# Optimization experiments

Hardware: AMD Instinct MI355X
Metric: run time of the kernel (lower is better)

Reference implementation:

```python
import jax, jax.numpy as jnp
import numpy as np

N, M, K, D = 65536, 131072, 8, 64
TAU = 0.3
EPS = 1e-6

def setup_inputs() -> dict:
    key = jax.random.key(0)
    ks = jax.random.split(key, 16)
    s = 0.05
    return {
        "f_pts": jax.random.normal(ks[0], (N, D), jnp.float32),
        "pts": jax.random.uniform(ks[1], (N, 3), jnp.float32) * 10.0,
        "z_latent": jax.random.normal(ks[2], (M, D), jnp.float32) * 0.1,
        "centers": jax.random.uniform(ks[3], (M, 3), jnp.float32) * 10.0,
        "cand_idx": jax.random.randint(ks[4], (N, K), 0, M),
        "sim_w1": jax.random.normal(ks[5], (2 * D + 3, 64), jnp.float32) * s,
        "sim_b1": jnp.zeros((64,), jnp.float32),
        "sim_w2": jax.random.normal(ks[6], (64, 1), jnp.float32) * s,
        "sim_b2": jnp.zeros((1,), jnp.float32),
        "gate_w1": jax.random.normal(ks[7], (2 * D, D), jnp.float32) * s,
        "gate_b1": jnp.zeros((D,), jnp.float32),
        "gate_w2": jax.random.normal(ks[8], (D, 1), jnp.float32) * s,
        "gate_b2": jnp.zeros((1,), jnp.float32),
        "W_ih": jax.random.normal(ks[9], (3 * D, D), jnp.float32) * s,
        "W_hh": jax.random.normal(ks[10], (3 * D, D), jnp.float32) * s,
        "b_ih": jnp.zeros((3 * D,), jnp.float32),
        "b_hh": jnp.zeros((3 * D,), jnp.float32),
    }

def _forward(f_pts, pts, z_latent, centers, sim_w1, sim_b1, sim_w2, sim_b2,
             gate_w1, gate_b1, gate_w2, gate_b2, W_ih, W_hh, b_ih, b_hh, cand_idx):
    n, k = cand_idx.shape
    m, d = z_latent.shape
    # --- gather voxel latents / centers for each (point, candidate) pair ---
    z_c = z_latent[cand_idx]                         # (N,K,D)
    delta = pts[:, None, :] - centers[cand_idx]      # (N,K,3)
    f_b = jnp.broadcast_to(f_pts[:, None, :], (n, k, d))
    # --- similarity MLP ---
    x = jnp.concatenate([f_b, z_c, delta], axis=-1)  # (N,K,2D+3)
    h = jax.nn.relu(x @ sim_w1 + sim_b1)
    sim = (h @ sim_w2 + sim_b2)[..., 0]              # (N,K)
    # --- low-temperature top-K routing weights over candidates ---
    w = jax.nn.softmax(sim / TAU, axis=-1)           # (N,K)
    # --- scatter weighted point features to voxels ---
    flat_idx = cand_idx.reshape(-1)                  # (N*K,)
    contrib = (w[..., None] * f_pts[:, None, :]).reshape(-1, d)
    msg = jax.ops.segment_sum(contrib, flat_idx, num_segments=m)     # (M,D)
    wsum = jax.ops.segment_sum(w.reshape(-1), flat_idx, num_segments=m)
    msg = msg / (wsum[:, None] + EPS)                # normalized voxel message
    # --- per-voxel gate ---
    g_in = jnp.concatenate([z_latent, msg], axis=-1)
    gate = jax.nn.sigmoid(jax.nn.relu(g_in @ gate_w1 + gate_b1) @ gate_w2 + gate_b2)  # (M,1)
    # --- GRUCell (torch layout: rows ordered r,z,n) ---
    gi = msg @ W_ih.T + b_ih
    gh = z_latent @ W_hh.T + b_hh
    i_r, i_z, i_n = jnp.split(gi, 3, axis=-1)
    h_r, h_z, h_n = jnp.split(gh, 3, axis=-1)
    r = jax.nn.sigmoid(i_r + h_r)
    zg = jax.nn.sigmoid(i_z + h_z)
    nn_ = jnp.tanh(i_n + r * h_n)
    h_new = (1.0 - zg) * nn_ + zg * z_latent
    # gated latent update
    return z_latent + gate * (h_new - z_latent)

def reference(f_pts, pts, z_latent, centers, cand_idx, sim_w1, sim_b1, sim_w2, sim_b2,
              gate_w1, gate_b1, gate_w2, gate_b2, W_ih, W_hh, b_ih, b_hh):
    return _forward(f_pts, pts, z_latent, centers, sim_w1, sim_b1, sim_w2, sim_b2,
                    gate_w1, gate_b1, gate_w2, gate_b2, W_ih, W_hh, b_ih, b_hh, cand_idx)
```

## Files before the change

### kernel.cpp

```cpp
#include <hip/hip_runtime.h>
#include <hip/hip_fp16.h>
#include <math.h>


typedef short bf16x8 __attribute__((ext_vector_type(8)));
typedef unsigned short u16x8 __attribute__((ext_vector_type(8)));
typedef float f32x4 __attribute__((ext_vector_type(4)));
#define MFMA __builtin_amdgcn_mfma_f32_16x16x32_bf16
#define CAP 32

__device__ __forceinline__ short f2bf(float f) {
  unsigned u = __float_as_uint(f);
  unsigned r = (u + 0x7FFFu + ((u >> 16) & 1u)) >> 16;
  return (short)r;
}

__device__ __forceinline__ float bf2f(unsigned short h) {
  return __uint_as_float(((unsigned)h) << 16);
}

__device__ __forceinline__ float sigm(float x) { return 1.0f / (1.0f + __expf(-x)); }

__global__ __launch_bounds__(256) void prep_kernel(
    const float* __restrict__ z, const float* __restrict__ f,
    const float* __restrict__ sim_w1, const float* __restrict__ sim_b1,
    unsigned short* __restrict__ zbf, unsigned short* __restrict__ fbf,
    unsigned short* __restrict__ HBt, int* __restrict__ cursor,
    short* __restrict__ bfZ, int M)
{
  long tid = (long)blockIdx.x * 256 + threadIdx.x;
  long nthr = (long)gridDim.x * 256;

  for (long i = tid; i < M; i += nthr) cursor[i] = 0;

  long nz = (long)M * 64;
  for (long i = tid * 8; i < nz; i += nthr * 8) {
    float4 a = *(const float4*)&z[i];
    float4 b4 = *(const float4*)&z[i + 4];
    u16x8 o;
    o[0] = (unsigned short)f2bf(a.x);  o[1] = (unsigned short)f2bf(a.y);
    o[2] = (unsigned short)f2bf(a.z);  o[3] = (unsigned short)f2bf(a.w);
    o[4] = (unsigned short)f2bf(b4.x); o[5] = (unsigned short)f2bf(b4.y);
    o[6] = (unsigned short)f2bf(b4.z); o[7] = (unsigned short)f2bf(b4.w);
    *(u16x8*)&zbf[i] = o;
  }

  if (blockIdx.x == gridDim.x - 1 && threadIdx.x < 64) {
    int lane = threadIdx.x;
    int lr = lane & 15, lg = lane >> 4;
#pragma unroll
    for (int ct = 0; ct < 4; ++ct)
#pragma unroll
      for (int kt = 0; kt < 3; ++kt) {
        bf16x8 b;
#pragma unroll
        for (int e = 0; e < 8; ++e) {
          int k = kt * 32 + lg * 8 + e;
          float v = (k < 67) ? sim_w1[(64 + k) * 64 + ct * 16 + lr] : 0.0f;
          b[e] = f2bf(v);
        }
        *(bf16x8*)&bfZ[(ct * 3 + kt) * 512 + lane * 8] = b;
      }
  }

  if (blockIdx.x < 1024) {
    int wave = blockIdx.x * 4 + (threadIdx.x >> 6);
    int lane = threadIdx.x & 63;
    int lr = lane & 15, lg = lane >> 4;
    int n0 = wave * 16;

    bf16x8 bf[8];
#pragma unroll
    for (int ct = 0; ct < 4; ++ct)
#pragma unroll
      for (int kt = 0; kt < 2; ++kt) {
        bf16x8 bb;
#pragma unroll
        for (int e = 0; e < 8; ++e)
          bb[e] = f2bf(sim_w1[(kt * 32 + lg * 8 + e) * 64 + ct * 16 + lr]);
        bf[ct * 2 + kt] = bb;
      }

    bf16x8 a[2];
#pragma unroll
    for (int kt = 0; kt < 2; ++kt) {
      const float* src = &f[(long)(n0 + lr) * 64 + kt * 32 + lg * 8];
      float4 v0 = *(const float4*)src;
      float4 v1 = *(const float4*)(src + 4);
      bf16x8 t;
      t[0] = f2bf(v0.x); t[1] = f2bf(v0.y); t[2] = f2bf(v0.z); t[3] = f2bf(v0.w);
      t[4] = f2bf(v1.x); t[5] = f2bf(v1.y); t[6] = f2bf(v1.z); t[7] = f2bf(v1.w);
      a[kt] = t;
    }
    *(bf16x8*)&fbf[(long)(n0 + lr) * 64 + lg * 8] = a[0];
    *(bf16x8*)&fbf[(long)(n0 + lr) * 64 + 32 + lg * 8] = a[1];

    f32x4 acc[4] = {{0,0,0,0},{0,0,0,0},{0,0,0,0},{0,0,0,0}};
#pragma unroll
    for (int ct = 0; ct < 4; ++ct) {
      acc[ct] = MFMA(a[0], bf[ct * 2 + 0], acc[ct], 0, 0, 0);
      acc[ct] = MFMA(a[1], bf[ct * 2 + 1], acc[ct], 0, 0, 0);
    }
    float b10 = sim_b1[lr], b11 = sim_b1[16 + lr];
    float b12 = sim_b1[32 + lr], b13 = sim_b1[48 + lr];
#pragma unroll
    for (int e = 0; e < 4; ++e) {
      unsigned lo = (unsigned)(unsigned short)f2bf(acc[0][e] + b10)
                  | ((unsigned)(unsigned short)f2bf(acc[1][e] + b11) << 16);
      unsigned hi = (unsigned)(unsigned short)f2bf(acc[2][e] + b12)
                  | ((unsigned)(unsigned short)f2bf(acc[3][e] + b13) << 16);
      *(uint2*)&HBt[(long)(n0 + lg * 4 + e) * 64 + lr * 4] = make_uint2(lo, hi);
    }
  }
}

#define TPW 8
__global__ __launch_bounds__(256) void pair_kernel(
    const float* __restrict__ pts, const unsigned short* __restrict__ zbf,
    const float* __restrict__ centers, const int* __restrict__ cand_idx,
    const float* __restrict__ sim_w2, const short* __restrict__ bfZ,
    const unsigned short* __restrict__ HBt,
    int* __restrict__ cursor, unsigned* __restrict__ rec)
{
  int wave = (blockIdx.x * 256 + threadIdx.x) >> 6;
  int lane = threadIdx.x & 63;
  int lr = lane & 15, lg = lane >> 4;

  int callA = cand_idx[wave * 128 + lane];
  int callB = cand_idx[wave * 128 + 64 + lane];
  int slotA = atomicAdd(&cursor[callA], 1);
  int slotB = atomicAdd(&cursor[callB], 1);

  bf16x8 b[12];
#pragma unroll
  for (int i = 0; i < 12; ++i) b[i] = *(const bf16x8*)&bfZ[i * 512 + lane * 8];
  float w2c[4];
#pragma unroll
  for (int ct = 0; ct < 4; ++ct) w2c[ct] = sim_w2[ct * 16 + lr];

  int c0 = __shfl(callA, lr, 64);
  bf16x8 a0 = *(const bf16x8*)&zbf[(long)c0 * 64 + lg * 8];
  bf16x8 a1 = *(const bf16x8*)&zbf[(long)c0 * 64 + 32 + lg * 8];
  float cx = 0, cy = 0, cz = 0, px = 0, py = 0, pz = 0;
  if (lg == 0) {
    cx = centers[c0 * 3 + 0]; cy = centers[c0 * 3 + 1]; cz = centers[c0 * 3 + 2];
    int n = wave * TPW * 2 + (lr >> 3);
    px = pts[n * 3 + 0]; py = pts[n * 3 + 1]; pz = pts[n * 3 + 2];
  }
  uint2 h2 = *(const uint2*)&HBt[((long)wave * TPW * 2 + (lg >> 1)) * 64 + lr * 4];

  float wst[TPW];

#pragma unroll
  for (int t = 0; t < TPW; ++t) {
    int cn = c0; bf16x8 an0 = a0, an1 = a1;
    float cxn = 0, cyn = 0, czn = 0, pxn = 0, pyn = 0, pzn = 0;
    uint2 h2n = make_uint2(0, 0);
    if (t + 1 < TPW) {
      cn = __shfl((t + 1) < 4 ? callA : callB, ((t + 1) & 3) * 16 + lr, 64);
      an0 = *(const bf16x8*)&zbf[(long)cn * 64 + lg * 8];
      an1 = *(const bf16x8*)&zbf[(long)cn * 64 + 32 + lg * 8];
      if (lg == 0) {
        cxn = centers[cn * 3 + 0]; cyn = centers[cn * 3 + 1]; czn = centers[cn * 3 + 2];
        int n = (wave * TPW + t + 1) * 2 + (lr >> 3);
        pxn = pts[n * 3 + 0]; pyn = pts[n * 3 + 1]; pzn = pts[n * 3 + 2];
      }
      h2n = *(const uint2*)&HBt[((long)(wave * TPW + t + 1) * 2 + (lg >> 1)) * 64 + lr * 4];
    }

    bf16x8 ad = {0, 0, 0, 0, 0, 0, 0, 0};
    if (lg == 0) {
      ad[0] = f2bf(px - cx); ad[1] = f2bf(py - cy); ad[2] = f2bf(pz - cz);
    }

    f32x4 acc[4] = {{0,0,0,0},{0,0,0,0},{0,0,0,0},{0,0,0,0}};
#pragma unroll
    for (int ct = 0; ct < 4; ++ct) {
      acc[ct] = MFMA(a0, b[ct * 3 + 0], acc[ct], 0, 0, 0);
      acc[ct] = MFMA(a1, b[ct * 3 + 1], acc[ct], 0, 0, 0);
      acc[ct] = MFMA(ad, b[ct * 3 + 2], acc[ct], 0, 0, 0);
    }

    float hb[4];
    hb[0] = bf2f((unsigned short)(h2.x));
    hb[1] = bf2f((unsigned short)(h2.x >> 16));
    hb[2] = bf2f((unsigned short)(h2.y));
    hb[3] = bf2f((unsigned short)(h2.y >> 16));

    f32x4 part = {0.f, 0.f, 0.f, 0.f};
#pragma unroll
    for (int ct = 0; ct < 4; ++ct)
#pragma unroll
      for (int e = 0; e < 4; ++e) {
        float u = fmaxf(acc[ct][e] + hb[ct], 0.0f);
        part[e] = fmaf(u, w2c[ct], part[e]);
      }
#pragma unroll
    for (int m = 1; m <= 8; m <<= 1)
#pragma unroll
      for (int e = 0; e < 4; ++e) part[e] += __shfl_xor(part[e], m, 64);

    float other[4];
#pragma unroll
    for (int e = 0; e < 4; ++e) other[e] = __shfl_xor(part[e], 16, 64);

    float mx = part[0];
#pragma unroll
    for (int e = 1; e < 4; ++e) mx = fmaxf(mx, part[e]);
#pragma unroll
    for (int e = 0; e < 4; ++e) mx = fmaxf(mx, other[e]);
    float ex[4], se = 0.f, so = 0.f;
#pragma unroll
    for (int e = 0; e < 4; ++e) {
      ex[e] = __expf((part[e] - mx) * (1.0f / 0.3f));
      se += ex[e];
      so += __expf((other[e] - mx) * (1.0f / 0.3f));
    }
    float inv = 1.0f / (se + so);

    int srcl = (lane >> 2) << 4;
    float t0 = __shfl(ex[0] * inv, srcl, 64);
    float t1 = __shfl(ex[1] * inv, srcl, 64);
    float t2 = __shfl(ex[2] * inv, srcl, 64);
    float t3 = __shfl(ex[3] * inv, srcl, 64);
    int esel = lane & 3;
    wst[t] = esel == 0 ? t0 : esel == 1 ? t1 : esel == 2 ? t2 : t3;

    c0 = cn; a0 = an0; a1 = an1;
    cx = cxn; cy = cyn; cz = czn; px = pxn; py = pyn; pz = pzn;
    h2 = h2n;
  }

  float v0 = __shfl(wst[0], lr, 64);
  float v1 = __shfl(wst[1], lr, 64);
  float v2 = __shfl(wst[2], lr, 64);
  float v3 = __shfl(wst[3], lr, 64);
  float v4 = __shfl(wst[4], lr, 64);
  float v5 = __shfl(wst[5], lr, 64);
  float v6 = __shfl(wst[6], lr, 64);
  float v7 = __shfl(wst[7], lr, 64);
  float wvA = lg == 0 ? v0 : lg == 1 ? v1 : lg == 2 ? v2 : v3;
  float wvB = lg == 0 ? v4 : lg == 1 ? v5 : lg == 2 ? v6 : v7;

  int base_pt = wave * 16 + 2 * lg + (lr >> 3);
  if (slotA < CAP) {
    unsigned short wh = __half_as_ushort(__float2half(wvA));
    rec[(long)callA * CAP + slotA] = ((unsigned)base_pt << 16) | (unsigned)wh;
  }
  if (slotB < CAP) {
    unsigned short wh = __half_as_ushort(__float2half(wvB));
    rec[(long)callB * CAP + slotB] = ((unsigned)(base_pt + 8) << 16) | (unsigned)wh;
  }
}

__global__ __launch_bounds__(256) void gather_kernel(
    const unsigned* __restrict__ rec, const int* __restrict__ cursor,
    const unsigned short* __restrict__ fbf, unsigned short* __restrict__ msg_bf,
    int mvox)
{
  int tid = blockIdx.x * 256 + threadIdx.x;
  int row = tid >> 2, seg = tid & 3;
  if (row >= mvox) return;

  int cnt = cursor[row];
  cnt = cnt < CAP ? cnt : CAP;
  const unsigned* rp = &rec[(long)row * CAP];

  float acc[16];
#pragma unroll
  for (int j = 0; j < 16; ++j) acc[j] = 0.f;
  float ws = 0.f;

  for (int i0 = 0; i0 < cnt; i0 += 4) {
    uint4 r4 = *(const uint4*)&rp[i0];
    unsigned rr0 = r4.x, rr1 = r4.y, rr2 = r4.z, rr3 = r4.w;
#pragma unroll
    for (int j = 0; j < 4; ++j) {
      unsigned r = j == 0 ? rr0 : j == 1 ? rr1 : j == 2 ? rr2 : rr3;
      if (i0 + j < cnt) {
        float w = __half2float(__ushort_as_half((unsigned short)(r & 0xffffu)));
        int n = r >> 16;
        ws += w;
        const u16x8* fp = (const u16x8*)&fbf[(long)n * 64 + seg * 16];
        u16x8 f0 = fp[0], f1 = fp[1];
#pragma unroll
        for (int k = 0; k < 8; ++k) {
          acc[k]     = fmaf(w, bf2f(f0[k]), acc[k]);
          acc[8 + k] = fmaf(w, bf2f(f1[k]), acc[8 + k]);
        }
      }
    }
  }
  float inv = 1.0f / (ws + 1e-6f);
  u16x8 o0, o1;
#pragma unroll
  for (int j = 0; j < 8; ++j) {
    o0[j] = (unsigned short)f2bf(acc[j] * inv);
    o1[j] = (unsigned short)f2bf(acc[8 + j] * inv);
  }
  *(u16x8*)&msg_bf[(long)row * 64 + seg * 16] = o0;
  *(u16x8*)&msg_bf[(long)row * 64 + seg * 16 + 8] = o1;
}

#define GST 136
#define WST 72

__global__ __launch_bounds__(512)
__attribute__((amdgpu_waves_per_eu(2, 2)))
void stage2(
    const unsigned short* __restrict__ zbf,
    const float* __restrict__ gate_w1, const float* __restrict__ gate_b1,
    const float* __restrict__ gate_w2, const float* __restrict__ gate_b2,
    const float* __restrict__ W_ih, const float* __restrict__ W_hh,
    const float* __restrict__ b_ih, const float* __restrict__ b_hh,
    const unsigned short* __restrict__ msg_bf,
    float* __restrict__ out, int ntiles)
{
  __shared__ short G1t[64 * GST];
  __shared__ short Wih_l[192 * WST];
  __shared__ short Whh_l[192 * WST];
  __shared__ float gb1s[64], gw2s[64], bihs[192], bhhs[192];
  __shared__ float gb2s;

  int t = threadIdx.x;
  for (int s = t; s < 64 * 128; s += 512) {
    int j = s & 63, k = s >> 6;
    G1t[j * GST + k] = f2bf(gate_w1[s]);
  }
  for (int s = t; s < 192 * 64; s += 512) {
    int j = s >> 6, k = s & 63;
    Wih_l[j * WST + k] = f2bf(W_ih[s]);
    Whh_l[j * WST + k] = f2bf(W_hh[s]);
  }
  if (t < 64) { gb1s[t] = gate_b1[t]; gw2s[t] = gate_w2[t]; }
  if (t < 192) { bihs[t] = b_ih[t]; bhhs[t] = b_hh[t]; }
  if (t == 0) gb2s = gate_b2[0];
  __syncthreads();

  int wid = t >> 6, lane = t & 63;
  int lr = lane & 15, lg = lane >> 4;

#pragma unroll 1
  for (int tile = blockIdx.x; tile < ntiles; tile += gridDim.x) {
    int rowbase = tile * 128 + wid * 16;
    long abase = (long)(rowbase + lr) * 64;
    bf16x8 a0 = *(const bf16x8*)&zbf[abase + lg * 8];
    bf16x8 a1 = *(const bf16x8*)&zbf[abase + 32 + lg * 8];
    bf16x8 a2 = *(const bf16x8*)&msg_bf[abase + lg * 8];
    bf16x8 a3 = *(const bf16x8*)&msg_bf[abase + 32 + lg * 8];

    f32x4 usum = {0.f, 0.f, 0.f, 0.f};
#pragma unroll 1
    for (int ct = 0; ct < 4; ++ct) {
      f32x4 au = {0, 0, 0, 0};
      au = MFMA(a0, *(const bf16x8*)&G1t[(ct * 16 + lr) * GST +  0 + lg * 8], au, 0, 0, 0);
      au = MFMA(a1, *(const bf16x8*)&G1t[(ct * 16 + lr) * GST + 32 + lg * 8], au, 0, 0, 0);
      au = MFMA(a2, *(const bf16x8*)&G1t[(ct * 16 + lr) * GST + 64 + lg * 8], au, 0, 0, 0);
      au = MFMA(a3, *(const bf16x8*)&G1t[(ct * 16 + lr) * GST + 96 + lg * 8], au, 0, 0, 0);
      int c = ct * 16 + lr;
#pragma unroll
      for (int e = 0; e < 4; ++e)
        usum[e] += fmaxf(au[e] + gb1s[c], 0.0f) * gw2s[c];
    }
#pragma unroll
    for (int m = 1; m <= 8; m <<= 1)
#pragma unroll
      for (int e = 0; e < 4; ++e) {
        float v = usum[e];
        usum[e] = v + __shfl_xor(v, m, 64);
      }
    float gate[4];
#pragma unroll
    for (int e = 0; e < 4; ++e) gate[e] = sigm(usum[e] + gb2s);

#pragma unroll 1
    for (int ct = 0; ct < 4; ++ct) {
      f32x4 air = {0,0,0,0}, aiz = {0,0,0,0}, ain = {0,0,0,0};
      f32x4 ahr = {0,0,0,0}, ahz = {0,0,0,0}, ahn = {0,0,0,0};
#pragma unroll
      for (int k2 = 0; k2 < 2; ++k2) {
        bf16x8 amg = k2 ? a3 : a2;
        bf16x8 az_ = k2 ? a1 : a0;
        int ko = k2 * 32 + lg * 8;
        air = MFMA(amg, *(const bf16x8*)&Wih_l[(      ct * 16 + lr) * WST + ko], air, 0, 0, 0);
        aiz = MFMA(amg, *(const bf16x8*)&Wih_l[( 64 + ct * 16 + lr) * WST + ko], aiz, 0, 0, 0);
        ain = MFMA(amg, *(const bf16x8*)&Wih_l[(128 + ct * 16 + lr) * WST + ko], ain, 0, 0, 0);
        ahr = MFMA(az_, *(const bf16x8*)&Whh_l[(      ct * 16 + lr) * WST + ko], ahr, 0, 0, 0);
        ahz = MFMA(az_, *(const bf16x8*)&Whh_l[( 64 + ct * 16 + lr) * WST + ko], ahz, 0, 0, 0);
        ahn = MFMA(az_, *(const bf16x8*)&Whh_l[(128 + ct * 16 + lr) * WST + ko], ahn, 0, 0, 0);
      }
      int c = ct * 16 + lr;
#pragma unroll
      for (int e = 0; e < 4; ++e) {
        float zv = bf2f(zbf[(long)(rowbase + lg * 4 + e) * 64 + c]);
        float rr = sigm(air[e] + bihs[c] + ahr[e] + bhhs[c]);
        float zg = sigm(aiz[e] + bihs[64 + c] + ahz[e] + bhhs[64 + c]);
        float nn = tanhf(ain[e] + bihs[128 + c] + rr * (ahn[e] + bhhs[128 + c]));
        float hnew = (1.0f - zg) * nn + zg * zv;
        out[(long)(rowbase + lg * 4 + e) * 64 + c] = zv + gate[e] * (hnew - zv);
      }
    }
  }
}

extern "C" void kernel_launch(void* const* d_in, const int* in_sizes, int n_in,
                              void* d_out, int out_size, void* d_ws, size_t ws_size,
                              hipStream_t stream) {
  const float* f_pts   = (const float*)d_in[0];
  const float* pts     = (const float*)d_in[1];
  const float* z_lat   = (const float*)d_in[2];
  const float* centers = (const float*)d_in[3];
  const int*   cand    = (const int*)d_in[4];
  const float* sim_w1  = (const float*)d_in[5];
  const float* sim_b1  = (const float*)d_in[6];
  const float* sim_w2  = (const float*)d_in[7];
  const float* gate_w1 = (const float*)d_in[9];
  const float* gate_b1 = (const float*)d_in[10];
  const float* gate_w2 = (const float*)d_in[11];
  const float* gate_b2 = (const float*)d_in[12];
  const float* W_ih    = (const float*)d_in[13];
  const float* W_hh    = (const float*)d_in[14];
  const float* b_ih    = (const float*)d_in[15];
  const float* b_hh    = (const float*)d_in[16];

  int N = in_sizes[0] / 64;
  int M = in_sizes[2] / 64;

  int* cursor = (int*)d_ws;
  unsigned* rec = (unsigned*)(cursor + M);
  unsigned short* msg_bf = (unsigned short*)rec;
  unsigned short* zbf = (unsigned short*)(rec + (size_t)M * CAP);
  unsigned short* fbf = zbf + (size_t)M * 64;
  unsigned short* HBt = fbf + (size_t)N * 64;
  short* bfZ = (short*)(HBt + (size_t)N * 64);

  prep_kernel<<<2048, 256, 0, stream>>>(z_lat, f_pts, sim_w1, sim_b1,
                                        zbf, fbf, HBt, cursor, bfZ, M);

  int nwaves = (N * 8) / (16 * TPW);
  pair_kernel<<<nwaves / 4, 256, 0, stream>>>(pts, zbf, centers, cand,
                                              sim_w2, bfZ, HBt, cursor, rec);

  gather_kernel<<<(M * 4) / 256, 256, 0, stream>>>(rec, cursor, fbf, msg_bf, M);

  int ntiles = M / 128;
  stage2<<<512, 512, 0, stream>>>(zbf, gate_w1, gate_b1, gate_w2, gate_b2,
                                  W_ih, W_hh, b_ih, b_hh, msg_bf,
                                  (float*)d_out, ntiles);
}
```

Baseline: 113.7 us.

## Fuse voxel gather into stage2 and halve pair-kernel tokens per wave

Removes the separate gather kernel and computes each voxel's normalized message inside stage2, directly in the MFMA A-operand layout. This avoids writing and re-reading msg_bf and saves one launch. The pair kernel now handles 4 tiles per wave instead of 8 and loads all of a wave's operands up front rather than software-pipelining them, which doubles the number of waves. The fused gather runs with less parallelism per row (one lane per 8 features, with 4 lanes per row within an MFMA layout), which risks longer latency chains inside stage2.

```diff
diff --git a/kernel.cpp b/kernel.cpp
--- a/kernel.cpp
+++ b/kernel.cpp
@@ -114,7 +114,7 @@
   }
 }
 
-#define TPW 8
+#define TPW 4
 __global__ __launch_bounds__(256) void pair_kernel(
     const float* __restrict__ pts, const unsigned short* __restrict__ zbf,
     const float* __restrict__ centers, const int* __restrict__ cand_idx,
@@ -126,10 +126,8 @@
   int lane = threadIdx.x & 63;
   int lr = lane & 15, lg = lane >> 4;
 
-  int callA = cand_idx[wave * 128 + lane];
-  int callB = cand_idx[wave * 128 + 64 + lane];
-  int slotA = atomicAdd(&cursor[callA], 1);
-  int slotB = atomicAdd(&cursor[callB], 1);
+  int call = cand_idx[wave * 64 + lane];
+  int slot = atomicAdd(&cursor[call], 1);
 
   bf16x8 b[12];
 #pragma unroll
@@ -138,168 +136,93 @@
 #pragma unroll
   for (int ct = 0; ct < 4; ++ct) w2c[ct] = sim_w2[ct * 16 + lr];
 
-  int c0 = __shfl(callA, lr, 64);
-  bf16x8 a0 = *(const bf16x8*)&zbf[(long)c0 * 64 + lg * 8];
-  bf16x8 a1 = *(const bf16x8*)&zbf[(long)c0 * 64 + 32 + lg * 8];
-  float cx = 0, cy = 0, cz = 0, px = 0, py = 0, pz = 0;
-  if (lg == 0) {
-    cx = centers[c0 * 3 + 0]; cy = centers[c0 * 3 + 1]; cz = centers[c0 * 3 + 2];
-    int n = wave * TPW * 2 + (lr >> 3);
-    px = pts[n * 3 + 0]; py = pts[n * 3 + 1]; pz = pts[n * 3 + 2];
-  }
-  uint2 h2 = *(const uint2*)&HBt[((long)wave * TPW * 2 + (lg >> 1)) * 64 + lr * 4];
-
-  float wst[TPW];
-
+  int c[TPW];
+  bf16x8 a0[TPW], a1[TPW], ad[TPW];
+  uint2 h2[TPW];
 #pragma unroll
   for (int t = 0; t < TPW; ++t) {
-    int cn = c0; bf16x8 an0 = a0, an1 = a1;
-    float cxn = 0, cyn = 0, czn = 0, pxn = 0, pyn = 0, pzn = 0;
-    uint2 h2n = make_uint2(0, 0);
-    if (t + 1 < TPW) {
-      cn = __shfl((t + 1) < 4 ? callA : callB, ((t + 1) & 3) * 16 + lr, 64);
-      an0 = *(const bf16x8*)&zbf[(long)cn * 64 + lg * 8];
-      an1 = *(const bf16x8*)&zbf[(long)cn * 64 + 32 + lg * 8];
-      if (lg == 0) {
-        cxn = centers[cn * 3 + 0]; cyn = centers[cn * 3 + 1]; czn = centers[cn * 3 + 2];
-        int n = (wave * TPW + t + 1) * 2 + (lr >> 3);
-        pxn = pts[n * 3 + 0]; pyn = pts[n * 3 + 1]; pzn = pts[n * 3 + 2];
-      }
-      h2n = *(const uint2*)&HBt[((long)(wave * TPW + t + 1) * 2 + (lg >> 1)) * 64 + lr * 4];
-    }
-
-    bf16x8 ad = {0, 0, 0, 0, 0, 0, 0, 0};
+    c[t] = __shfl(call, t * 16 + lr, 64);
+    a0[t] = *(const bf16x8*)&zbf[(long)c[t] * 64 + lg * 8];
+    a1[t] = *(const bf16x8*)&zbf[(long)c[t] * 64 + 32 + lg * 8];
+    h2[t] = *(const uint2*)&HBt[((long)(wave * TPW + t) * 2 + (lg >> 1)) * 64 + lr * 4];
+    bf16x8 tt = {0, 0, 0, 0, 0, 0, 0, 0};
     if (lg == 0) {
-      ad[0] = f2bf(px - cx); ad[1] = f2bf(py - cy); ad[2] = f2bf(pz - cz);
-    }
-
+      int n = (wave * TPW + t) * 2 + (lr >> 3);
+      tt[0] = f2bf(pts[n * 3 + 0] - centers[c[t] * 3 + 0]);
+      tt[1] = f2bf(pts[n * 3 + 1] - centers[c[t] * 3 + 1]);
+      tt[2] = f2bf(pts[n * 3 + 2] - centers[c[t] * 3 + 2]);
+    }
+    ad[t] = tt;
+  }
+
+  f32x4 part[TPW];
+#pragma unroll
+  for (int t = 0; t < TPW; ++t) {
     f32x4 acc[4] = {{0,0,0,0},{0,0,0,0},{0,0,0,0},{0,0,0,0}};
 #pragma unroll
     for (int ct = 0; ct < 4; ++ct) {
-      acc[ct] = MFMA(a0, b[ct * 3 + 0], acc[ct], 0, 0, 0);
-      acc[ct] = MFMA(a1, b[ct * 3 + 1], acc[ct], 0, 0, 0);
-      acc[ct] = MFMA(ad, b[ct * 3 + 2], acc[ct], 0, 0, 0);
-    }
-
+      acc[ct] = MFMA(a0[t], b[ct * 3 + 0], acc[ct], 0, 0, 0);
+      acc[ct] = MFMA(a1[t], b[ct * 3 + 1], acc[ct], 0, 0, 0);
+      acc[ct] = MFMA(ad[t], b[ct * 3 + 2], acc[ct], 0, 0, 0);
+    }
     float hb[4];
-    hb[0] = bf2f((unsigned short)(h2.x));
-    hb[1] = bf2f((unsigned short)(h2.x >> 16));
-    hb[2] = bf2f((unsigned short)(h2.y));
-    hb[3] = bf2f((unsigned short)(h2.y >> 16));
-
-    f32x4 part = {0.f, 0.f, 0.f, 0.f};
+    hb[0] = bf2f((unsigned short)(h2[t].x));
+    hb[1] = bf2f((unsigned short)(h2[t].x >> 16));
+    hb[2] = bf2f((unsigned short)(h2[t].y));
+    hb[3] = bf2f((unsigned short)(h2[t].y >> 16));
+    f32x4 p = {0.f, 0.f, 0.f, 0.f};
 #pragma unroll
     for (int ct = 0; ct < 4; ++ct)
 #pragma unroll
-      for (int e = 0; e < 4; ++e) {
-        float u = fmaxf(acc[ct][e] + hb[ct], 0.0f);
-        part[e] = fmaf(u, w2c[ct], part[e]);
-      }
+      for (int e = 0; e < 4; ++e)
+        p[e] = fmaf(fmaxf(acc[ct][e] + hb[ct], 0.0f), w2c[ct], p[e]);
+    part[t] = p;
+  }
+
+  float wrow[TPW];
+#pragma unroll
+  for (int t = 0; t < TPW; ++t) {
+    f32x4 p = part[t];
 #pragma unroll
     for (int m = 1; m <= 8; m <<= 1)
 #pragma unroll
-      for (int e = 0; e < 4; ++e) part[e] += __shfl_xor(part[e], m, 64);
-
+      for (int e = 0; e < 4; ++e) p[e] += __shfl_xor(p[e], m, 64);
     float other[4];
 #pragma unroll
-    for (int e = 0; e < 4; ++e) other[e] = __shfl_xor(part[e], 16, 64);
-
-    float mx = part[0];
-#pragma unroll
-    for (int e = 1; e < 4; ++e) mx = fmaxf(mx, part[e]);
+    for (int e = 0; e < 4; ++e) other[e] = __shfl_xor(p[e], 16, 64);
+    float mx = p[0];
+#pragma unroll
+    for (int e = 1; e < 4; ++e) mx = fmaxf(mx, p[e]);
 #pragma unroll
     for (int e = 0; e < 4; ++e) mx = fmaxf(mx, other[e]);
     float ex[4], se = 0.f, so = 0.f;
 #pragma unroll
     for (int e = 0; e < 4; ++e) {
-      ex[e] = __expf((part[e] - mx) * (1.0f / 0.3f));
+      ex[e] = __expf((p[e] - mx) * (1.0f / 0.3f));
       se += ex[e];
       so += __expf((other[e] - mx) * (1.0f / 0.3f));
     }
     float inv = 1.0f / (se + so);
-
     int srcl = (lane >> 2) << 4;
     float t0 = __shfl(ex[0] * inv, srcl, 64);
     float t1 = __shfl(ex[1] * inv, srcl, 64);
     float t2 = __shfl(ex[2] * inv, srcl, 64);
     float t3 = __shfl(ex[3] * inv, srcl, 64);
     int esel = lane & 3;
-    wst[t] = esel == 0 ? t0 : esel == 1 ? t1 : esel == 2 ? t2 : t3;
-
-    c0 = cn; a0 = an0; a1 = an1;
-    cx = cxn; cy = cyn; cz = czn; px = pxn; py = pyn; pz = pzn;
-    h2 = h2n;
-  }
-
-  float v0 = __shfl(wst[0], lr, 64);
-  float v1 = __shfl(wst[1], lr, 64);
-  float v2 = __shfl(wst[2], lr, 64);
-  float v3 = __shfl(wst[3], lr, 64);
-  float v4 = __shfl(wst[4], lr, 64);
-  float v5 = __shfl(wst[5], lr, 64);
-  float v6 = __shfl(wst[6], lr, 64);
-  float v7 = __shfl(wst[7], lr, 64);
-  float wvA = lg == 0 ? v0 : lg == 1 ? v1 : lg == 2 ? v2 : v3;
-  float wvB = lg == 0 ? v4 : lg == 1 ? v5 : lg == 2 ? v6 : v7;
-
-  int base_pt = wave * 16 + 2 * lg + (lr >> 3);
-  if (slotA < CAP) {
-    unsigned short wh = __half_as_ushort(__float2half(wvA));
-    rec[(long)callA * CAP + slotA] = ((unsigned)base_pt << 16) | (unsigned)wh;
-  }
-  if (slotB < CAP) {
-    unsigned short wh = __half_as_ushort(__float2half(wvB));
-    rec[(long)callB * CAP + slotB] = ((unsigned)(base_pt + 8) << 16) | (unsigned)wh;
-  }
-}
-
-__global__ __launch_bounds__(256) void gather_kernel(
-    const unsigned* __restrict__ rec, const int* __restrict__ cursor,
-    const unsigned short* __restrict__ fbf, unsigned short* __restrict__ msg_bf,
-    int mvox)
-{
-  int tid = blockIdx.x * 256 + threadIdx.x;
-  int row = tid >> 2, seg = tid & 3;
-  if (row >= mvox) return;
-
-  int cnt = cursor[row];
-  cnt = cnt < CAP ? cnt : CAP;
-  const unsigned* rp = &rec[(long)row * CAP];
-
-  float acc[16];
-#pragma unroll
-  for (int j = 0; j < 16; ++j) acc[j] = 0.f;
-  float ws = 0.f;
-
-  for (int i0 = 0; i0 < cnt; i0 += 4) {
-    uint4 r4 = *(const uint4*)&rp[i0];
-    unsigned rr0 = r4.x, rr1 = r4.y, rr2 = r4.z, rr3 = r4.w;
-#pragma unroll
-    for (int j = 0; j < 4; ++j) {
-      unsigned r = j == 0 ? rr0 : j == 1 ? rr1 : j == 2 ? rr2 : rr3;
-      if (i0 + j < cnt) {
-        float w = __half2float(__ushort_as_half((unsigned short)(r & 0xffffu)));
-        int n = r >> 16;
-        ws += w;
-        const u16x8* fp = (const u16x8*)&fbf[(long)n * 64 + seg * 16];
-        u16x8 f0 = fp[0], f1 = fp[1];
-#pragma unroll
-        for (int k = 0; k < 8; ++k) {
-          acc[k]     = fmaf(w, bf2f(f0[k]), acc[k]);
-          acc[8 + k] = fmaf(w, bf2f(f1[k]), acc[8 + k]);
-        }
-      }
-    }
-  }
-  float inv = 1.0f / (ws + 1e-6f);
-  u16x8 o0, o1;
-#pragma unroll
-  for (int j = 0; j < 8; ++j) {
-    o0[j] = (unsigned short)f2bf(acc[j] * inv);
-    o1[j] = (unsigned short)f2bf(acc[8 + j] * inv);
-  }
-  *(u16x8*)&msg_bf[(long)row * 64 + seg * 16] = o0;
-  *(u16x8*)&msg_bf[(long)row * 64 + seg * 16 + 8] = o1;
+    wrow[t] = esel == 0 ? t0 : esel == 1 ? t1 : esel == 2 ? t2 : t3;
+  }
+
+  float v0 = __shfl(wrow[0], lr, 64);
+  float v1 = __shfl(wrow[1], lr, 64);
+  float v2 = __shfl(wrow[2], lr, 64);
+  float v3 = __shfl(wrow[3], lr, 64);
+  float wv = lg == 0 ? v0 : lg == 1 ? v1 : lg == 2 ? v2 : v3;
+
+  if (slot < CAP) {
+    int n_pt = wave * 8 + 2 * lg + (lr >> 3);
+    unsigned short wh = __half_as_ushort(__float2half(wv));
+    rec[(long)call * CAP + slot] = ((unsigned)n_pt << 16) | (unsigned)wh;
+  }
 }
 
 #define GST 136
@@ -313,7 +236,8 @@
     const float* __restrict__ gate_w2, const float* __restrict__ gate_b2,
     const float* __restrict__ W_ih, const float* __restrict__ W_hh,
     const float* __restrict__ b_ih, const float* __restrict__ b_hh,
-    const unsigned short* __restrict__ msg_bf,
+    const unsigned* __restrict__ rec, const int* __restrict__ cursor,
+    const unsigned short* __restrict__ fbf,
     float* __restrict__ out, int ntiles)
 {
   __shared__ short G1t[64 * GST];
@@ -343,11 +267,45 @@
 #pragma unroll 1
   for (int tile = blockIdx.x; tile < ntiles; tile += gridDim.x) {
     int rowbase = tile * 128 + wid * 16;
-    long abase = (long)(rowbase + lr) * 64;
+    int myrow = rowbase + lr;
+    long abase = (long)myrow * 64;
     bf16x8 a0 = *(const bf16x8*)&zbf[abase + lg * 8];
     bf16x8 a1 = *(const bf16x8*)&zbf[abase + 32 + lg * 8];
-    bf16x8 a2 = *(const bf16x8*)&msg_bf[abase + lg * 8];
-    bf16x8 a3 = *(const bf16x8*)&msg_bf[abase + 32 + lg * 8];
+
+    int cnt = cursor[myrow];
+    cnt = cnt < CAP ? cnt : CAP;
+    const unsigned* rp = &rec[(long)myrow * CAP];
+    float accA[8], accB[8];
+#pragma unroll
+    for (int k = 0; k < 8; ++k) { accA[k] = 0.f; accB[k] = 0.f; }
+    float ws = 0.f;
+#pragma unroll 1
+    for (int i0 = 0; i0 < cnt; i0 += 4) {
+      uint4 r4 = *(const uint4*)&rp[i0];
+#pragma unroll
+      for (int j = 0; j < 4; ++j) {
+        unsigned r = j == 0 ? r4.x : j == 1 ? r4.y : j == 2 ? r4.z : r4.w;
+        if (i0 + j < cnt) {
+          float w = __half2float(__ushort_as_half((unsigned short)(r & 0xffffu)));
+          int n = r >> 16;
+          ws += w;
+          u16x8 fA = *(const u16x8*)&fbf[(long)n * 64 + lg * 8];
+          u16x8 fB = *(const u16x8*)&fbf[(long)n * 64 + 32 + lg * 8];
+#pragma unroll
+          for (int k = 0; k < 8; ++k) {
+            accA[k] = fmaf(w, bf2f(fA[k]), accA[k]);
+            accB[k] = fmaf(w, bf2f(fB[k]), accB[k]);
+          }
+        }
+      }
+    }
+    float minv = 1.0f / (ws + 1e-6f);
+    bf16x8 a2, a3;
+#pragma unroll
+    for (int k = 0; k < 8; ++k) {
+      a2[k] = f2bf(accA[k] * minv);
+      a3[k] = f2bf(accB[k] * minv);
+    }
 
     f32x4 usum = {0.f, 0.f, 0.f, 0.f};
 #pragma unroll 1
@@ -428,7 +386,6 @@
 
   int* cursor = (int*)d_ws;
   unsigned* rec = (unsigned*)(cursor + M);
-  unsigned short* msg_bf = (unsigned short*)rec;
   unsigned short* zbf = (unsigned short*)(rec + (size_t)M * CAP);
   unsigned short* fbf = zbf + (size_t)M * 64;
   unsigned short* HBt = fbf + (size_t)N * 64;
@@ -441,10 +398,8 @@
   pair_kernel<<<nwaves / 4, 256, 0, stream>>>(pts, zbf, centers, cand,
                                               sim_w2, bfZ, HBt, cursor, rec);
 
-  gather_kernel<<<(M * 4) / 256, 256, 0, stream>>>(rec, cursor, fbf, msg_bf, M);
-
   int ntiles = M / 128;
   stage2<<<512, 512, 0, stream>>>(zbf, gate_w1, gate_b1, gate_w2, gate_b2,
-                                  W_ih, W_hh, b_ih, b_hh, msg_bf,
+                                  W_ih, W_hh, b_ih, b_hh, rec, cursor, fbf,
                                   (float*)d_out, ntiles);
 }
```

Measured after the change: 112.0 us. Within noise of the previous version (-1.5%).
